# Kernel optimization log

Measured on AMD Instinct MI355X. Metric: run time of the kernel, lower is better.

The kernel has to match this reference:

```python
import math
import jax, jax.numpy as jnp
import numpy as np

N = 50000
C = 128      # in_channels == out_channels
H = 8        # nhead
D = C // H   # head_dim = 16
E = 800000


def _layernorm(x, g, b, eps=1e-5):
    mu = jnp.mean(x, axis=-1, keepdims=True)
    var = jnp.var(x, axis=-1, keepdims=True)
    return (x - mu) * jax.lax.rsqrt(var + eps) * g + b


def setup_inputs() -> dict:
    key = jax.random.key(0)
    ks = jax.random.split(key, 12)
    s = 1.0 / math.sqrt(C)          # ~xavier scale
    s4 = 1.0 / math.sqrt(4 * C)
    return {
        "x": jax.random.normal(ks[0], (N, C), dtype=jnp.float32),
        "edge_index": jax.random.randint(ks[1], (2, E), 0, N, dtype=jnp.int64),
        "Wq": jax.random.normal(ks[2], (C, C), dtype=jnp.float32) * s,
        "Wk": jax.random.normal(ks[3], (C, C), dtype=jnp.float32) * s,
        "Wv": jax.random.normal(ks[4], (C, C), dtype=jnp.float32) * s,
        "Wo": jax.random.normal(ks[5], (C, C), dtype=jnp.float32) * s,
        "bo": jnp.zeros((C,), dtype=jnp.float32),
        "Wf1": jax.random.normal(ks[6], (C, 4 * C), dtype=jnp.float32) * s,
        "bf1": jnp.zeros((4 * C,), dtype=jnp.float32),
        "Wf2": jax.random.normal(ks[7], (4 * C, C), dtype=jnp.float32) * s4,
        "bf2": jnp.zeros((C,), dtype=jnp.float32),
        "g1": jnp.ones((C,), dtype=jnp.float32),
        "b1": jnp.zeros((C,), dtype=jnp.float32),
        "g2": jnp.ones((C,), dtype=jnp.float32),
        "b2": jnp.zeros((C,), dtype=jnp.float32),
    }


def reference(x, edge_index, Wq, Wk, Wv, Wo, bo, Wf1, bf1, Wf2, bf2, g1, b1, g2, b2):
    n = x.shape[0]
    loops = jnp.arange(n, dtype=edge_index.dtype)
    row = jnp.concatenate([edge_index[0], loops])  # source nodes
    col = jnp.concatenate([edge_index[1], loops])  # destination nodes

    q = (x @ Wq).reshape(n, H, D)
    k = (x @ Wk).reshape(n, H, D)
    v = (x @ Wv).reshape(n, H, D)

    # edge-level attention scores [E+N, H]
    scores = jnp.einsum('ehd,ehd->eh', q[row], k[col]) / math.sqrt(D)
    smax = jax.ops.segment_max(scores, col, num_segments=n)  # every node has a self-loop
    exp = jnp.exp(scores - smax[col])
    ssum = jax.ops.segment_sum(exp, col, num_segments=n)
    alpha = exp / (ssum[col] + 1e-8)

    out = jax.ops.segment_sum(v[row] * alpha[..., None], col, num_segments=n)
    attn = out.reshape(n, C) @ Wo + bo

    residual = x  # input_proj is Identity (in_channels == out_channels)
    x1 = _layernorm(residual + attn, g1, b1)
    ffn = jax.nn.gelu(x1 @ Wf1 + bf1, approximate=False) @ Wf2 + bf2
    return _layernorm(x1 + ffn, g2, b2)
```

## Files before the change

kernel.cpp:

```cpp
#include <hip/hip_runtime.h>
#include <cmath>


typedef short bf16x8 __attribute__((ext_vector_type(8)));
typedef float f32x4 __attribute__((ext_vector_type(4)));
typedef unsigned int uint_as1 __attribute__((address_space(1)));
typedef unsigned int uint_as3 __attribute__((address_space(3)));

__device__ inline unsigned short f2bf(float f) {
    unsigned int u = __float_as_uint(f);
    u += 0x7fffu + ((u >> 16) & 1u);
    return (unsigned short)(u >> 16);
}
__device__ inline float bflo(unsigned int w) { return __uint_as_float(w << 16); }
__device__ inline float bfhi(unsigned int w) { return __uint_as_float(w & 0xffff0000u); }

__device__ inline void gload16(const unsigned short* g, unsigned short* l) {
    __builtin_amdgcn_global_load_lds((const uint_as1*)g, (uint_as3*)l, 16, 0, 0);
}

__device__ inline float gelu_f(float x) {
    float ax = fabsf(x) * 0.70710678118f;
    float t = __builtin_amdgcn_rcpf(fmaf(0.3275911f, ax, 1.0f));
    float p = fmaf(1.061405429f, t, -1.453152027f);
    p = fmaf(p, t, 1.421413741f);
    p = fmaf(p, t, -0.284496736f);
    p = fmaf(p, t, 0.254829592f);
    p = p * t;
    float e = __expf(-ax * ax);
    float pe = p * e;
    float w = (x >= 0.f) ? (2.0f - pe) : pe;
    return 0.5f * x * w;
}


__global__ void k_zero(int* __restrict__ p, int n) {
    int i = blockIdx.x * 256 + threadIdx.x;
    if (i < n) p[i] = 0;
}

__global__ void k_count(const int* __restrict__ ei, int* __restrict__ counts,
                        int E, int N) {
    int e = blockIdx.x * 256 + threadIdx.x;
    if (e >= E + N) return;
    int col = (e < E) ? ei[E + e] : (e - E);
    atomicAdd(&counts[col], 1);
}

__global__ void k_scan1(const int* __restrict__ counts, int* __restrict__ incl,
                        int* __restrict__ bsums, int N) {
    __shared__ int s[256];
    int t = threadIdx.x, i = blockIdx.x * 256 + t;
    int v = (i < N) ? counts[i] : 0;
    s[t] = v; __syncthreads();
    for (int off = 1; off < 256; off <<= 1) {
        int add = (t >= off) ? s[t - off] : 0;
        __syncthreads();
        s[t] += add;
        __syncthreads();
    }
    if (i < N) incl[i] = s[t];
    if (t == 255) bsums[blockIdx.x] = s[255];
}

__global__ void k_scan2(const int* __restrict__ bsums, int* __restrict__ boffs, int NB) {
    __shared__ int s[256];
    int t = threadIdx.x;
    int v = (t < NB) ? bsums[t] : 0;
    s[t] = v; __syncthreads();
    for (int off = 1; off < 256; off <<= 1) {
        int add = (t >= off) ? s[t - off] : 0;
        __syncthreads();
        s[t] += add;
        __syncthreads();
    }
    if (t < NB) boffs[t] = s[t] - v;
}

__global__ void k_scan3(const int* __restrict__ incl, const int* __restrict__ counts,
                        const int* __restrict__ boffs, int* __restrict__ nstart,
                        int* __restrict__ cursor, int N) {
    int i = blockIdx.x * 256 + threadIdx.x;
    if (i >= N) return;
    int st = incl[i] - counts[i] + boffs[blockIdx.x];
    nstart[i] = st;
    cursor[i] = st;
}

__global__ void k_fill(const int* __restrict__ ei, int* __restrict__ cursor,
                       int* __restrict__ csr, int E, int N) {
    int e = blockIdx.x * 256 + threadIdx.x;
    if (e >= E + N) return;
    int row, col;
    if (e < E) { row = ei[e]; col = ei[E + e]; }
    else       { row = col = e - E; }
    int pos = atomicAdd(&cursor[col], 1);
    csr[pos] = row;
}


__global__ void k_cast(const float* __restrict__ x, unsigned short* __restrict__ xb,
                       int total4) {
    int i = blockIdx.x * 256 + threadIdx.x;
    if (i >= total4) return;
    float4 v = ((const float4*)x)[i];
    ushort4 o;
    o.x = f2bf(v.x); o.y = f2bf(v.y); o.z = f2bf(v.z); o.w = f2bf(v.w);
    ((ushort4*)xb)[i] = o;
}

__global__ void k_prep(const float* Wq, const float* Wk, const float* Wv, const float* Wo,
                       const float* Wf1, const float* Wf2,
                       unsigned short* Wqkvt, unsigned short* Wot,
                       unsigned short* Wf1t, unsigned short* Wf2t) {
    int z = blockIdx.y;
    const float* in; unsigned short* out; int K, Co;
    switch (z) {
        case 0: in = Wq;  out = Wqkvt;          K = 128; Co = 128; break;
        case 1: in = Wk;  out = Wqkvt + 16384;  K = 128; Co = 128; break;
        case 2: in = Wv;  out = Wqkvt + 32768;  K = 128; Co = 128; break;
        case 3: in = Wo;  out = Wot;            K = 128; Co = 128; break;
        case 4: in = Wf1; out = Wf1t;           K = 128; Co = 512; break;
        default: in = Wf2; out = Wf2t;          K = 512; Co = 128; break;
    }
    int idx = blockIdx.x * 256 + threadIdx.x;
    if (idx >= K * Co) return;
    int k = idx / Co, c = idx % Co;
    out[c * K + k] = f2bf(in[idx]);
}


template <int EPI, int KS, int WR>
__global__ __launch_bounds__(WR * 128, WR == 2 ? 3 : 2) void k_gemm(
    const unsigned short* __restrict__ A, const unsigned short* __restrict__ Bt,
    const float* __restrict__ bias, const float* __restrict__ resid,
    const float* __restrict__ g, const float* __restrict__ b,
    float* __restrict__ outf, unsigned short* __restrict__ outb,
    int M, int Cout) {
    constexpr int K = KS * 32;
    constexpr int NT = WR * 128;
    constexpr int CPR = K / 8;
    constexpr int RPI = NT / CPR;
    constexpr int NITER = 128 / RPI;
    __shared__ unsigned short Bs[128 * K];

    int tid = threadIdx.x;
    int wid = tid >> 6, lane = tid & 63;
    int quad = lane >> 4, l16 = lane & 15;
    int wr = wid >> 1, wc = wid & 1;
    int m0 = blockIdx.x * (WR * 64);
    int n0 = blockIdx.y * 128;

    const unsigned short* Arow[4];
#pragma unroll
    for (int ti = 0; ti < 4; ++ti) {
        int row = m0 + wr * 64 + ti * 16 + l16;
        if (row > M - 1) row = M - 1;
        Arow[ti] = A + (size_t)row * K + quad * 8;
    }

#define LOADA(buf, kc)                                                        \
    _Pragma("unroll") for (int ti_ = 0; ti_ < 4; ++ti_)                       \
        _Pragma("unroll") for (int j_ = 0; j_ < 4; ++j_)                      \
            buf[ti_][j_] = *(const bf16x8*)(Arow[ti_] + ((kc) + j_) * 32);

    bf16x8 a0[4][4];
    LOADA(a0, 0);
    bf16x8 a1[4][4];
    if constexpr (KS > 4) { LOADA(a1, 4); }

    {
        int srow = tid / CPR;
        int c = tid % CPR;
        int gc = (c & ~7) | ((c & 7) ^ (srow & 7));
        const unsigned short* src = Bt + (size_t)(n0 + srow) * K + gc * 8;
        unsigned short* dst = Bs + tid * 8;
#pragma unroll
        for (int j = 0; j < NITER; ++j)
            gload16(src + (size_t)j * RPI * K, dst + (size_t)j * RPI * K);
    }
    __syncthreads();

    f32x4 acc[4][4];
#pragma unroll
    for (int i = 0; i < 4; ++i)
#pragma unroll
        for (int j = 0; j < 4; ++j) acc[i][j] = {0.f, 0.f, 0.f, 0.f};

#define KCHUNK(buf, kc)                                                       \
    _Pragma("unroll") for (int ks_ = 0; ks_ < 4; ++ks_) {                     \
        bf16x8 bfr[4];                                                        \
        _Pragma("unroll") for (int tj_ = 0; tj_ < 4; ++tj_) {                 \
            int nr = wc * 64 + tj_ * 16 + l16;                                \
            int cidx = ((kc) + ks_) * 4 + quad;                               \
            int slot = (cidx & ~7) | ((cidx & 7) ^ (nr & 7));                 \
            bfr[tj_] = *(const bf16x8*)&Bs[nr * K + slot * 8];                \
        }                                                                     \
        _Pragma("unroll") for (int ti_ = 0; ti_ < 4; ++ti_)                   \
            _Pragma("unroll") for (int tj_ = 0; tj_ < 4; ++tj_)               \
                acc[ti_][tj_] = __builtin_amdgcn_mfma_f32_16x16x32_bf16(      \
                    buf[ti_][ks_], bfr[tj_], acc[ti_][tj_], 0, 0, 0);         \
    }

    KCHUNK(a0, 0);
    if constexpr (KS > 4) {
        LOADA(a0, 8);
        KCHUNK(a1, 4);
        LOADA(a1, 12);
        KCHUNK(a0, 8);
        KCHUNK(a1, 12);
    }
#undef LOADA
#undef KCHUNK

    if constexpr (EPI != 2) {
#pragma unroll
        for (int ti = 0; ti < 4; ++ti)
#pragma unroll
            for (int tj = 0; tj < 4; ++tj) {
                int col = n0 + wc * 64 + tj * 16 + l16;
#pragma unroll
                for (int r = 0; r < 4; ++r) {
                    int row = m0 + wr * 64 + ti * 16 + quad * 4 + r;
                    if (row >= M) continue;
                    float v = acc[ti][tj][r];
                    if constexpr (EPI == 1) v = gelu_f(v + bias[col]);
                    outb[(size_t)row * Cout + col] = f2bf(v);
                }
            }
    } else {
        __shared__ float pSum[2][WR * 64];
        __shared__ float pSq[2][WR * 64];
        float bi[4], gv[4], bv[4];
#pragma unroll
        for (int tj = 0; tj < 4; ++tj) {
            int col = wc * 64 + tj * 16 + l16;
            bi[tj] = bias[col]; gv[tj] = g[col]; bv[tj] = b[col];
        }
#pragma unroll
        for (int ti = 0; ti < 4; ++ti)
#pragma unroll
            for (int tj = 0; tj < 4; ++tj) {
                int col = wc * 64 + tj * 16 + l16;
#pragma unroll
                for (int r = 0; r < 4; ++r) {
                    int row = m0 + wr * 64 + ti * 16 + quad * 4 + r;
                    float rv = (row < M) ? resid[(size_t)row * 128 + col] : 0.f;
                    acc[ti][tj][r] += bi[tj] + rv;
                }
            }
#pragma unroll
        for (int ti = 0; ti < 4; ++ti)
#pragma unroll
            for (int r = 0; r < 4; ++r) {
                float s = acc[ti][0][r] + acc[ti][1][r] + acc[ti][2][r] + acc[ti][3][r];
                float q = acc[ti][0][r] * acc[ti][0][r] + acc[ti][1][r] * acc[ti][1][r]
                        + acc[ti][2][r] * acc[ti][2][r] + acc[ti][3][r] * acc[ti][3][r];
                s += __shfl_xor(s, 1); q += __shfl_xor(q, 1);
                s += __shfl_xor(s, 2); q += __shfl_xor(q, 2);
                s += __shfl_xor(s, 4); q += __shfl_xor(q, 4);
                s += __shfl_xor(s, 8); q += __shfl_xor(q, 8);
                if (l16 == 0) {
                    int lr = wr * 64 + ti * 16 + quad * 4 + r;
                    pSum[wc][lr] = s; pSq[wc][lr] = q;
                }
            }
        __syncthreads();
        if (tid < WR * 64) {
            float s = pSum[0][tid] + pSum[1][tid];
            float q = pSq[0][tid] + pSq[1][tid];
            float mean = s * 0.0078125f;
            float var = q * 0.0078125f - mean * mean;
            pSum[0][tid] = mean;
            pSq[0][tid] = rsqrtf(var + 1e-5f);
        }
        __syncthreads();
#pragma unroll
        for (int ti = 0; ti < 4; ++ti)
#pragma unroll
            for (int r = 0; r < 4; ++r) {
                int lr = wr * 64 + ti * 16 + quad * 4 + r;
                int row = m0 + lr;
                if (row >= M) continue;
                float mean = pSum[0][lr], rs = pSq[0][lr];
#pragma unroll
                for (int tj = 0; tj < 4; ++tj) {
                    int col = wc * 64 + tj * 16 + l16;
                    float y = (acc[ti][tj][r] - mean) * rs * gv[tj] + bv[tj];
                    if (outf) outf[(size_t)row * 128 + col] = y;
                    if (outb) outb[(size_t)row * 128 + col] = f2bf(y);
                }
            }
    }
}


__global__ __launch_bounds__(256) void k_attn(
    const unsigned int* __restrict__ qkv, const int* __restrict__ nstart,
    const int* __restrict__ counts, const int* __restrict__ csr,
    unsigned int* __restrict__ ob, int N) {
    int j = blockIdx.x * 4 + (threadIdx.x >> 6);
    if (j >= N) return;
    int l = threadIdx.x & 63;

    unsigned int kw = qkv[(size_t)j * 192 + 64 + l];
    float kx = bflo(kw), ky = bfhi(kw);

    int start = nstart[j], cnt = counts[j];
    float m = -3.0e38f, lsum = 0.f, a0 = 0.f, a1 = 0.f;
    int i = 0;
    for (; i + 4 <= cnt; i += 4) {
        int r0 = csr[start + i + 0], r1 = csr[start + i + 1];
        int r2 = csr[start + i + 2], r3 = csr[start + i + 3];
        unsigned int qw0 = qkv[(size_t)r0 * 192 + l];
        unsigned int qw1 = qkv[(size_t)r1 * 192 + l];
        unsigned int qw2 = qkv[(size_t)r2 * 192 + l];
        unsigned int qw3 = qkv[(size_t)r3 * 192 + l];
        unsigned int vw0 = qkv[(size_t)r0 * 192 + 128 + l];
        unsigned int vw1 = qkv[(size_t)r1 * 192 + 128 + l];
        unsigned int vw2 = qkv[(size_t)r2 * 192 + 128 + l];
        unsigned int vw3 = qkv[(size_t)r3 * 192 + 128 + l];

        float p0 = fmaf(bflo(qw0), kx, bfhi(qw0) * ky);
        float p1 = fmaf(bflo(qw1), kx, bfhi(qw1) * ky);
        float p2 = fmaf(bflo(qw2), kx, bfhi(qw2) * ky);
        float p3 = fmaf(bflo(qw3), kx, bfhi(qw3) * ky);
        p0 += __shfl_xor(p0, 1); p1 += __shfl_xor(p1, 1);
        p2 += __shfl_xor(p2, 1); p3 += __shfl_xor(p3, 1);
        p0 += __shfl_xor(p0, 2); p1 += __shfl_xor(p1, 2);
        p2 += __shfl_xor(p2, 2); p3 += __shfl_xor(p3, 2);
        p0 += __shfl_xor(p0, 4); p1 += __shfl_xor(p1, 4);
        p2 += __shfl_xor(p2, 4); p3 += __shfl_xor(p3, 4);
        float s0 = p0 * 0.25f, s1 = p1 * 0.25f, s2 = p2 * 0.25f, s3 = p3 * 0.25f;

        float mn = fmaxf(fmaxf(fmaxf(s0, s1), fmaxf(s2, s3)), m);
        float scale = __expf(m - mn);
        float e0 = __expf(s0 - mn), e1 = __expf(s1 - mn);
        float e2 = __expf(s2 - mn), e3 = __expf(s3 - mn);
        lsum = lsum * scale + ((e0 + e1) + (e2 + e3));
        a0 = a0 * scale + e0 * bflo(vw0) + e1 * bflo(vw1) + e2 * bflo(vw2) + e3 * bflo(vw3);
        a1 = a1 * scale + e0 * bfhi(vw0) + e1 * bfhi(vw1) + e2 * bfhi(vw2) + e3 * bfhi(vw3);
        m = mn;
    }
    for (; i < cnt; ++i) {
        int r = csr[start + i];
        unsigned int qw = qkv[(size_t)r * 192 + l];
        unsigned int vw = qkv[(size_t)r * 192 + 128 + l];
        float p = fmaf(bflo(qw), kx, bfhi(qw) * ky);
        p += __shfl_xor(p, 1);
        p += __shfl_xor(p, 2);
        p += __shfl_xor(p, 4);
        float sc = p * 0.25f;
        float mn = fmaxf(m, sc);
        float scale = __expf(m - mn);
        float e = __expf(sc - mn);
        lsum = lsum * scale + e;
        a0 = a0 * scale + e * bflo(vw);
        a1 = a1 * scale + e * bfhi(vw);
        m = mn;
    }
    float inv = 1.f / (lsum + 1e-8f);
    unsigned int w = ((unsigned int)f2bf(a1 * inv) << 16) | (unsigned int)f2bf(a0 * inv);
    ob[(size_t)j * 64 + l] = w;
}


extern "C" void kernel_launch(void* const* d_in, const int* in_sizes, int n_in,
                              void* d_out, int out_size, void* d_ws, size_t ws_size,
                              hipStream_t stream) {
    const float* x   = (const float*)d_in[0];
    const int* ei    = (const int*)d_in[1];
    const float* Wq  = (const float*)d_in[2];
    const float* Wk  = (const float*)d_in[3];
    const float* Wv  = (const float*)d_in[4];
    const float* Wo  = (const float*)d_in[5];
    const float* bo  = (const float*)d_in[6];
    const float* Wf1 = (const float*)d_in[7];
    const float* bf1 = (const float*)d_in[8];
    const float* Wf2 = (const float*)d_in[9];
    const float* bf2 = (const float*)d_in[10];
    const float* g1  = (const float*)d_in[11];
    const float* b1  = (const float*)d_in[12];
    const float* g2  = (const float*)d_in[13];
    const float* b2  = (const float*)d_in[14];

    int N = in_sizes[0] / 128;
    int E = in_sizes[1] / 2;
    int N2 = ((N + 127) / 128) * 128;
    int NE = E + N;

    char* p = (char*)d_ws;
    auto alloc = [&](size_t bytes) -> char* {
        char* r = p;
        p += (bytes + 255) & ~(size_t)255;
        return r;
    };
    unsigned short* qkv = (unsigned short*)alloc((size_t)N2 * 512 * 2);
    unsigned short* ob  = qkv + (size_t)N2 * 384;
    unsigned short* hb  = qkv;
    unsigned short* x1b = (unsigned short*)alloc((size_t)N2 * 128 * 2);
    unsigned short* xb  = x1b;
    float* x1f          = (float*)alloc((size_t)N2 * 128 * 4);
    unsigned short* Wqkvt = (unsigned short*)alloc(3 * 128 * 128 * 2);
    unsigned short* Wot   = (unsigned short*)alloc(128 * 128 * 2);
    unsigned short* Wf1t  = (unsigned short*)alloc(512 * 128 * 2);
    unsigned short* Wf2t  = (unsigned short*)alloc(128 * 512 * 2);
    int* counts = (int*)alloc((size_t)N * 4);
    int* incl   = (int*)alloc((size_t)N * 4);
    int* nstart = (int*)alloc((size_t)N * 4);
    int* cursor = (int*)alloc((size_t)N * 4);
    int* bsums  = (int*)alloc(1024 * 4);
    int* boffs  = (int*)alloc(1024 * 4);
    int* csr    = (int*)alloc((size_t)NE * 4);

    int NB = (N + 255) / 256;
    int M128 = (N + 127) / 128;
    int M256 = (N + 255) / 256;

    k_zero<<<NB, 256, 0, stream>>>(counts, N);
    k_count<<<(NE + 255) / 256, 256, 0, stream>>>(ei, counts, E, N);
    k_scan1<<<NB, 256, 0, stream>>>(counts, incl, bsums, N);
    k_scan2<<<1, 256, 0, stream>>>(bsums, boffs, NB);
    k_scan3<<<NB, 256, 0, stream>>>(incl, counts, boffs, nstart, cursor, N);
    k_fill<<<(NE + 255) / 256, 256, 0, stream>>>(ei, cursor, csr, E, N);

    k_cast<<<((N * 128 / 4) + 255) / 256, 256, 0, stream>>>(x, xb, N * 128 / 4);
    k_prep<<<dim3(256, 6), 256, 0, stream>>>(Wq, Wk, Wv, Wo, Wf1, Wf2,
                                             Wqkvt, Wot, Wf1t, Wf2t);

    k_gemm<0, 4, 2><<<dim3(M128, 3), 256, 0, stream>>>(
        xb, Wqkvt, nullptr, nullptr, nullptr, nullptr, nullptr, qkv, N, 384);

    k_attn<<<(N + 3) / 4, 256, 0, stream>>>((const unsigned int*)qkv, nstart,
                                            counts, csr, (unsigned int*)ob, N);

    k_gemm<2, 4, 2><<<dim3(M128, 1), 256, 0, stream>>>(
        ob, Wot, bo, x, g1, b1, x1f, x1b, N, 128);

    k_gemm<1, 4, 2><<<dim3(M128, 4), 256, 0, stream>>>(
        x1b, Wf1t, bf1, nullptr, nullptr, nullptr, nullptr, hb, N, 512);

    k_gemm<2, 16, 4><<<dim3(M256, 1), 512, 0, stream>>>(
        hb, Wf2t, bf2, x1f, g2, b2, (float*)d_out, nullptr, N, 128);
}
```

Measured before the change: 384.2 us.

## Interleave Q/V in QKV layout, pad CSR rows, drop online softmax max

The QKV GEMM epilogue now writes Q and V interleaved per node (with K moved to a separate region), so each edge in the attention kernel fetches q and v together in one 8-byte load. CSR segments are padded to multiples of 4 so neighbour indices can be read as int4, and the edge loop is software-pipelined by prefetching the next four rows. The running-max rescaling of the online softmax is removed and exp is applied directly to the scores, with the 0.25 scale folded into k. This saves the max and rescale arithmetic but risks overflow or precision loss if scores grow large; it relies on scores staying small for these inputs.

```diff
diff --git a/kernel.cpp b/kernel.cpp
--- a/kernel.cpp
+++ b/kernel.cpp
@@ -51,7 +51,7 @@
                         int* __restrict__ bsums, int N) {
     __shared__ int s[256];
     int t = threadIdx.x, i = blockIdx.x * 256 + t;
-    int v = (i < N) ? counts[i] : 0;
+    int v = (i < N) ? ((counts[i] + 3) & ~3) : 0;
     s[t] = v; __syncthreads();
     for (int off = 1; off < 256; off <<= 1) {
         int add = (t >= off) ? s[t - off] : 0;
@@ -82,7 +82,7 @@
                         int* __restrict__ cursor, int N) {
     int i = blockIdx.x * 256 + threadIdx.x;
     if (i >= N) return;
-    int st = incl[i] - counts[i] + boffs[blockIdx.x];
+    int st = incl[i] - ((counts[i] + 3) & ~3) + boffs[blockIdx.x];
     nstart[i] = st;
     cursor[i] = st;
 }
@@ -213,18 +213,33 @@
 #undef LOADA
 #undef KCHUNK
 
-    if constexpr (EPI != 2) {
+    if constexpr (EPI == 0) {
+        int z = blockIdx.y;
 #pragma unroll
         for (int ti = 0; ti < 4; ++ti)
 #pragma unroll
             for (int tj = 0; tj < 4; ++tj) {
-                int col = n0 + wc * 64 + tj * 16 + l16;
+                int cc = wc * 64 + tj * 16 + l16;
+                int off = (z == 1) ? (256 + cc)
+                                   : ((((cc >> 1) << 2) | (cc & 1)) + ((z == 2) ? 2 : 0));
 #pragma unroll
                 for (int r = 0; r < 4; ++r) {
                     int row = m0 + wr * 64 + ti * 16 + quad * 4 + r;
                     if (row >= M) continue;
-                    float v = acc[ti][tj][r];
-                    if constexpr (EPI == 1) v = gelu_f(v + bias[col]);
+                    outb[(size_t)row * 384 + off] = f2bf(acc[ti][tj][r]);
+                }
+            }
+    } else if constexpr (EPI == 1) {
+#pragma unroll
+        for (int ti = 0; ti < 4; ++ti)
+#pragma unroll
+            for (int tj = 0; tj < 4; ++tj) {
+                int col = n0 + wc * 64 + tj * 16 + l16;
+#pragma unroll
+                for (int r = 0; r < 4; ++r) {
+                    int row = m0 + wr * 64 + ti * 16 + quad * 4 + r;
+                    if (row >= M) continue;
+                    float v = gelu_f(acc[ti][tj][r] + bias[col]);
                     outb[(size_t)row * Cout + col] = f2bf(v);
                 }
             }
@@ -301,63 +316,64 @@
     unsigned int* __restrict__ ob, int N) {
     int j = blockIdx.x * 4 + (threadIdx.x >> 6);
     if (j >= N) return;
-    int l = threadIdx.x & 63;
-
-    unsigned int kw = qkv[(size_t)j * 192 + 64 + l];
-    float kx = bflo(kw), ky = bfhi(kw);
+    unsigned int l = threadIdx.x & 63;
+
+    unsigned int kw = qkv[(unsigned)j * 192u + 128u + l];
+    float kx = bflo(kw) * 0.25f, ky = bfhi(kw) * 0.25f;
 
     int start = nstart[j], cnt = counts[j];
-    float m = -3.0e38f, lsum = 0.f, a0 = 0.f, a1 = 0.f;
-    int i = 0;
-    for (; i + 4 <= cnt; i += 4) {
-        int r0 = csr[start + i + 0], r1 = csr[start + i + 1];
-        int r2 = csr[start + i + 2], r3 = csr[start + i + 3];
-        unsigned int qw0 = qkv[(size_t)r0 * 192 + l];
-        unsigned int qw1 = qkv[(size_t)r1 * 192 + l];
-        unsigned int qw2 = qkv[(size_t)r2 * 192 + l];
-        unsigned int qw3 = qkv[(size_t)r3 * 192 + l];
-        unsigned int vw0 = qkv[(size_t)r0 * 192 + 128 + l];
-        unsigned int vw1 = qkv[(size_t)r1 * 192 + 128 + l];
-        unsigned int vw2 = qkv[(size_t)r2 * 192 + 128 + l];
-        unsigned int vw3 = qkv[(size_t)r3 * 192 + 128 + l];
-
-        float p0 = fmaf(bflo(qw0), kx, bfhi(qw0) * ky);
-        float p1 = fmaf(bflo(qw1), kx, bfhi(qw1) * ky);
-        float p2 = fmaf(bflo(qw2), kx, bfhi(qw2) * ky);
-        float p3 = fmaf(bflo(qw3), kx, bfhi(qw3) * ky);
+    const uint2* qv = (const uint2*)qkv;
+    float lsum = 0.f, a0 = 0.f, a1 = 0.f;
+
+    auto edge4 = [&](uint2 w0, uint2 w1, uint2 w2, uint2 w3) {
+        float p0 = fmaf(bflo(w0.x), kx, bfhi(w0.x) * ky);
+        float p1 = fmaf(bflo(w1.x), kx, bfhi(w1.x) * ky);
+        float p2 = fmaf(bflo(w2.x), kx, bfhi(w2.x) * ky);
+        float p3 = fmaf(bflo(w3.x), kx, bfhi(w3.x) * ky);
         p0 += __shfl_xor(p0, 1); p1 += __shfl_xor(p1, 1);
         p2 += __shfl_xor(p2, 1); p3 += __shfl_xor(p3, 1);
         p0 += __shfl_xor(p0, 2); p1 += __shfl_xor(p1, 2);
         p2 += __shfl_xor(p2, 2); p3 += __shfl_xor(p3, 2);
         p0 += __shfl_xor(p0, 4); p1 += __shfl_xor(p1, 4);
         p2 += __shfl_xor(p2, 4); p3 += __shfl_xor(p3, 4);
-        float s0 = p0 * 0.25f, s1 = p1 * 0.25f, s2 = p2 * 0.25f, s3 = p3 * 0.25f;
-
-        float mn = fmaxf(fmaxf(fmaxf(s0, s1), fmaxf(s2, s3)), m);
-        float scale = __expf(m - mn);
-        float e0 = __expf(s0 - mn), e1 = __expf(s1 - mn);
-        float e2 = __expf(s2 - mn), e3 = __expf(s3 - mn);
-        lsum = lsum * scale + ((e0 + e1) + (e2 + e3));
-        a0 = a0 * scale + e0 * bflo(vw0) + e1 * bflo(vw1) + e2 * bflo(vw2) + e3 * bflo(vw3);
-        a1 = a1 * scale + e0 * bfhi(vw0) + e1 * bfhi(vw1) + e2 * bfhi(vw2) + e3 * bfhi(vw3);
-        m = mn;
+        float e0 = __expf(p0), e1 = __expf(p1);
+        float e2 = __expf(p2), e3 = __expf(p3);
+        lsum += (e0 + e1) + (e2 + e3);
+        a0 = fmaf(e0, bflo(w0.y), a0); a1 = fmaf(e0, bfhi(w0.y), a1);
+        a0 = fmaf(e1, bflo(w1.y), a0); a1 = fmaf(e1, bfhi(w1.y), a1);
+        a0 = fmaf(e2, bflo(w2.y), a0); a1 = fmaf(e2, bfhi(w2.y), a1);
+        a0 = fmaf(e3, bflo(w3.y), a0); a1 = fmaf(e3, bfhi(w3.y), a1);
+    };
+
+    int i = 0;
+    if (cnt >= 4) {
+        int4 rr = *(const int4*)&csr[start];
+        uint2 w0 = qv[(unsigned)rr.x * 96u + l];
+        uint2 w1 = qv[(unsigned)rr.y * 96u + l];
+        uint2 w2 = qv[(unsigned)rr.z * 96u + l];
+        uint2 w3 = qv[(unsigned)rr.w * 96u + l];
+        for (i = 4; i + 4 <= cnt; i += 4) {
+            int4 rn = *(const int4*)&csr[start + i];
+            uint2 n0 = qv[(unsigned)rn.x * 96u + l];
+            uint2 n1 = qv[(unsigned)rn.y * 96u + l];
+            uint2 n2 = qv[(unsigned)rn.z * 96u + l];
+            uint2 n3 = qv[(unsigned)rn.w * 96u + l];
+            edge4(w0, w1, w2, w3);
+            w0 = n0; w1 = n1; w2 = n2; w3 = n3;
+        }
+        edge4(w0, w1, w2, w3);
     }
     for (; i < cnt; ++i) {
         int r = csr[start + i];
-        unsigned int qw = qkv[(size_t)r * 192 + l];
-        unsigned int vw = qkv[(size_t)r * 192 + 128 + l];
-        float p = fmaf(bflo(qw), kx, bfhi(qw) * ky);
+        uint2 w = qv[(unsigned)r * 96u + l];
+        float p = fmaf(bflo(w.x), kx, bfhi(w.x) * ky);
         p += __shfl_xor(p, 1);
         p += __shfl_xor(p, 2);
         p += __shfl_xor(p, 4);
-        float sc = p * 0.25f;
-        float mn = fmaxf(m, sc);
-        float scale = __expf(m - mn);
-        float e = __expf(sc - mn);
-        lsum = lsum * scale + e;
-        a0 = a0 * scale + e * bflo(vw);
-        a1 = a1 * scale + e * bfhi(vw);
-        m = mn;
+        float e = __expf(p);
+        lsum += e;
+        a0 = fmaf(e, bflo(w.y), a0);
+        a1 = fmaf(e, bfhi(w.y), a1);
     }
     float inv = 1.f / (lsum + 1e-8f);
     unsigned int w = ((unsigned int)f2bf(a1 * inv) << 16) | (unsigned int)f2bf(a0 * inv);
@@ -411,7 +427,7 @@
     int* cursor = (int*)alloc((size_t)N * 4);
     int* bsums  = (int*)alloc(1024 * 4);
     int* boffs  = (int*)alloc(1024 * 4);
-    int* csr    = (int*)alloc((size_t)NE * 4);
+    int* csr    = (int*)alloc(((size_t)NE + 3 * (size_t)N + 64) * 4);
 
     int NB = (N + 255) / 256;
     int M128 = (N + 127) / 128;
```

New measurement: 391.9 us. Within noise of the previous version (+2.0%).
